# Optimization experiments

Measured on AMD Instinct MI355X. Metric: run time of the kernel, lower is better.

## Reference

```python
import jax, jax.numpy as jnp
import numpy as np

# KernelRnn.slow_update for one converted parameter, time_lag_covariance=None path:
#   var <- variance_update / time_index - mean_update**2
#   update = concat([mean_update, var], axis=0)            # [2R, m, n]
#   val = Q @ update (contract rule axis)                  # [C,  m, n]
#   new_chemical = y*chemical + z*(tanh(K_slow @ chemical) + val)
#   h = v @ new_chemical                                   # [m, n]

C = 5       # numberOfSlowChemicals
R = 14      # numberUpdateRules (all rules enabled)
M, N = 2048, 1024  # underlying weight matrix shape


def setup_inputs() -> dict:
    key = jax.random.key(0)
    ks = jax.random.split(key, 8)
    chemical = jax.random.normal(ks[0], (C, M, N), dtype=jnp.float32)
    mean_update = jax.random.normal(ks[1], (R, M, N), dtype=jnp.float32)
    variance_update = jax.random.uniform(ks[2], (R, M, N), dtype=jnp.float32)
    Q = jax.random.normal(ks[3], (C, 2 * R), dtype=jnp.float32) * 0.01
    K_slow = jax.random.normal(ks[4], (C, C), dtype=jnp.float32) * 0.01
    v = jnp.ones((1, C), dtype=jnp.float32) / C
    # tau-spaced decay vectors as in init_slow_params
    min_tau, max_tau = 2.0, 50.0
    tau = min_tau * (max_tau / min_tau) ** jnp.linspace(0.0, 1.0, C)
    z = (1.0 / tau).astype(jnp.float32)
    y = (1.0 - z).astype(jnp.float32)
    return {
        "chemical": chemical,
        "mean_update": mean_update,
        "variance_update": variance_update,
        "Q": Q,
        "K_slow": K_slow,
        "v": v,
        "y": y,
        "z": z,
        "time_index": 10,
    }


def reference(chemical, mean_update, variance_update, Q, K_slow, v, y, z, time_index):
    inv_t = 1.0 / jnp.asarray(time_index, dtype=chemical.dtype)
    var = variance_update * inv_t - mean_update * mean_update        # [R, m, n]
    update = jnp.concatenate([mean_update, var], axis=0)             # [2R, m, n]
    val = jnp.einsum('cr,rmn->cmn', Q, update)                       # [C, m, n]
    mixed = jnp.tanh(jnp.einsum('cd,dmn->cmn', K_slow, chemical))    # [C, m, n]
    new_chemical = (y[:, None, None] * chemical
                    + z[:, None, None] * (mixed + val))              # [C, m, n]
    h = jnp.einsum('oc,cmn->omn', v, new_chemical)[0]                # [m, n]
    return h
```

## Files before the change

### kernel.cpp

```cpp
#include <hip/hip_runtime.h>


#define CC 5
#define RR 14

__global__ void prep_kernel(const float* __restrict__ Q,
                            const float* __restrict__ Ks,
                            const float* __restrict__ v,
                            const float* __restrict__ y,
                            const float* __restrict__ z,
                            const int* __restrict__ tindex,
                            float* __restrict__ cf) {
    int i = threadIdx.x;
    float inv_t = 1.0f / (float)tindex[0];
    if (i < RR) {
        float a = 0.0f, b = 0.0f;
        #pragma unroll
        for (int c = 0; c < CC; ++c) {
            float vz = v[c] * z[c];
            a = fmaf(vz, Q[c * (2 * RR) + i], a);
            b = fmaf(vz, Q[c * (2 * RR) + RR + i], b);
        }
        cf[i] = a;
        cf[16 + i] = b * inv_t;
        cf[32 + i] = b;
    } else if (i < RR + CC) {
        int c = i - RR;
        cf[48 + c] = v[c] * y[c];
        cf[53 + c] = v[c] * z[c];
    } else if (i < RR + CC + CC * CC) {
        int j = i - (RR + CC);
        cf[58 + j] = Ks[j];
    }
}

__device__ __forceinline__ float fast_tanh(float x) {
    float e = __expf(2.0f * x);
    return fmaf(-2.0f, __builtin_amdgcn_rcpf(e + 1.0f), 1.0f);
}

__global__ __launch_bounds__(256)
void fused_kernel(const float* __restrict__ chem,
                  const float* __restrict__ meanu,
                  const float* __restrict__ varu,
                  const float* __restrict__ cf,
                  float* __restrict__ out,
                  int P) {
    int t = blockIdx.x * blockDim.x + threadIdx.x;
    int p = t * 4;
    if (p >= P) return;

    float4 ch[CC];
    #pragma unroll
    for (int c = 0; c < CC; ++c)
        ch[c] = *reinterpret_cast<const float4*>(chem + (size_t)c * P + p);

    float4 acc = make_float4(0.f, 0.f, 0.f, 0.f);
    #pragma unroll
    for (int c = 0; c < CC; ++c) {
        float vy = cf[48 + c];
        acc.x = fmaf(vy, ch[c].x, acc.x);
        acc.y = fmaf(vy, ch[c].y, acc.y);
        acc.z = fmaf(vy, ch[c].z, acc.z);
        acc.w = fmaf(vy, ch[c].w, acc.w);
    }

    #pragma unroll
    for (int c = 0; c < CC; ++c) {
        float4 s = make_float4(0.f, 0.f, 0.f, 0.f);
        #pragma unroll
        for (int d = 0; d < CC; ++d) {
            float k = cf[58 + c * CC + d];
            s.x = fmaf(k, ch[d].x, s.x);
            s.y = fmaf(k, ch[d].y, s.y);
            s.z = fmaf(k, ch[d].z, s.z);
            s.w = fmaf(k, ch[d].w, s.w);
        }
        float vz = cf[53 + c];
        acc.x = fmaf(vz, fast_tanh(s.x), acc.x);
        acc.y = fmaf(vz, fast_tanh(s.y), acc.y);
        acc.z = fmaf(vz, fast_tanh(s.z), acc.z);
        acc.w = fmaf(vz, fast_tanh(s.w), acc.w);
    }

    #pragma unroll
    for (int r = 0; r < RR; ++r) {
        float4 mu = *reinterpret_cast<const float4*>(meanu + (size_t)r * P + p);
        float4 va = *reinterpret_cast<const float4*>(varu + (size_t)r * P + p);
        float ar = cf[r], bir = cf[16 + r], br = cf[32 + r];
        acc.x = fmaf(ar, mu.x, acc.x);
        acc.y = fmaf(ar, mu.y, acc.y);
        acc.z = fmaf(ar, mu.z, acc.z);
        acc.w = fmaf(ar, mu.w, acc.w);
        acc.x = fmaf(bir, va.x, acc.x);
        acc.y = fmaf(bir, va.y, acc.y);
        acc.z = fmaf(bir, va.z, acc.z);
        acc.w = fmaf(bir, va.w, acc.w);
        acc.x = fmaf(-br, mu.x * mu.x, acc.x);
        acc.y = fmaf(-br, mu.y * mu.y, acc.y);
        acc.z = fmaf(-br, mu.z * mu.z, acc.z);
        acc.w = fmaf(-br, mu.w * mu.w, acc.w);
    }

    *reinterpret_cast<float4*>(out + p) = acc;
}

extern "C" void kernel_launch(void* const* d_in, const int* in_sizes, int n_in,
                              void* d_out, int out_size, void* d_ws, size_t ws_size,
                              hipStream_t stream) {
    const float* chem  = (const float*)d_in[0];
    const float* meanu = (const float*)d_in[1];
    const float* varu  = (const float*)d_in[2];
    const float* Q     = (const float*)d_in[3];
    const float* Ks    = (const float*)d_in[4];
    const float* v     = (const float*)d_in[5];
    const float* y     = (const float*)d_in[6];
    const float* z     = (const float*)d_in[7];
    const int*   ti    = (const int*)d_in[8];

    float* cf = (float*)d_ws;
    float* out = (float*)d_out;

    prep_kernel<<<1, 64, 0, stream>>>(Q, Ks, v, y, z, ti, cf);

    int P = out_size;
    int nthreads = (P + 3) / 4;
    int blocks = (nthreads + 255) / 256;
    fused_kernel<<<blocks, 256, 0, stream>>>(chem, meanu, varu, cf, out, P);
}
```

Baseline: 299.5 us.

## Process two float4 per thread with a rolled update-rule loop

Each thread now handles two float4 vectors, strided by blockDim, and loops over update rules without unrolling. The mean and variance streams are read before the chemical tensor. This is meant to cut register pressure and raise occupancy while keeping coalesced loads. Fewer loads are in flight per thread, and the bounds check is gone, so it relies on P being a multiple of the tile size.

```diff
diff --git a/kernel.cpp b/kernel.cpp
--- a/kernel.cpp
+++ b/kernel.cpp
@@ -3,6 +3,7 @@
 
 #define CC 5
 #define RR 14
+#define VU 2
 
 __global__ void prep_kernel(const float* __restrict__ Q,
                             const float* __restrict__ Ks,
@@ -46,63 +47,80 @@
                   const float* __restrict__ cf,
                   float* __restrict__ out,
                   int P) {
-    int t = blockIdx.x * blockDim.x + threadIdx.x;
-    int p = t * 4;
-    if (p >= P) return;
+    const int tid = threadIdx.x;
+    const size_t tile = (size_t)blockIdx.x * (256 * VU * 4);
 
-    float4 ch[CC];
+    float4 acc[VU];
     #pragma unroll
-    for (int c = 0; c < CC; ++c)
-        ch[c] = *reinterpret_cast<const float4*>(chem + (size_t)c * P + p);
+    for (int u = 0; u < VU; ++u) acc[u] = make_float4(0.f, 0.f, 0.f, 0.f);
 
-    float4 acc = make_float4(0.f, 0.f, 0.f, 0.f);
+    #pragma unroll 1
+    for (int r = 0; r < RR; ++r) {
+        const float4* pm = reinterpret_cast<const float4*>(meanu + (size_t)r * P + tile);
+        const float4* pv = reinterpret_cast<const float4*>(varu  + (size_t)r * P + tile);
+        float4 m[VU], w[VU];
+        #pragma unroll
+        for (int u = 0; u < VU; ++u) m[u] = pm[u * 256 + tid];
+        #pragma unroll
+        for (int u = 0; u < VU; ++u) w[u] = pv[u * 256 + tid];
+        float ar = cf[r], bir = cf[16 + r], br = cf[32 + r];
+        #pragma unroll
+        for (int u = 0; u < VU; ++u) {
+            acc[u].x = fmaf(ar, m[u].x, acc[u].x);
+            acc[u].y = fmaf(ar, m[u].y, acc[u].y);
+            acc[u].z = fmaf(ar, m[u].z, acc[u].z);
+            acc[u].w = fmaf(ar, m[u].w, acc[u].w);
+            acc[u].x = fmaf(bir, w[u].x, acc[u].x);
+            acc[u].y = fmaf(bir, w[u].y, acc[u].y);
+            acc[u].z = fmaf(bir, w[u].z, acc[u].z);
+            acc[u].w = fmaf(bir, w[u].w, acc[u].w);
+            acc[u].x = fmaf(-br, m[u].x * m[u].x, acc[u].x);
+            acc[u].y = fmaf(-br, m[u].y * m[u].y, acc[u].y);
+            acc[u].z = fmaf(-br, m[u].z * m[u].z, acc[u].z);
+            acc[u].w = fmaf(-br, m[u].w * m[u].w, acc[u].w);
+        }
+    }
+
+    float4 ch[CC][VU];
     #pragma unroll
     for (int c = 0; c < CC; ++c) {
-        float vy = cf[48 + c];
-        acc.x = fmaf(vy, ch[c].x, acc.x);
-        acc.y = fmaf(vy, ch[c].y, acc.y);
-        acc.z = fmaf(vy, ch[c].z, acc.z);
-        acc.w = fmaf(vy, ch[c].w, acc.w);
+        const float4* pc = reinterpret_cast<const float4*>(chem + (size_t)c * P + tile);
+        #pragma unroll
+        for (int u = 0; u < VU; ++u) ch[c][u] = pc[u * 256 + tid];
     }
 
     #pragma unroll
-    for (int c = 0; c < CC; ++c) {
-        float4 s = make_float4(0.f, 0.f, 0.f, 0.f);
+    for (int u = 0; u < VU; ++u) {
         #pragma unroll
-        for (int d = 0; d < CC; ++d) {
-            float k = cf[58 + c * CC + d];
-            s.x = fmaf(k, ch[d].x, s.x);
-            s.y = fmaf(k, ch[d].y, s.y);
-            s.z = fmaf(k, ch[d].z, s.z);
-            s.w = fmaf(k, ch[d].w, s.w);
+        for (int c = 0; c < CC; ++c) {
+            float vy = cf[48 + c];
+            acc[u].x = fmaf(vy, ch[c][u].x, acc[u].x);
+            acc[u].y = fmaf(vy, ch[c][u].y, acc[u].y);
+            acc[u].z = fmaf(vy, ch[c][u].z, acc[u].z);
+            acc[u].w = fmaf(vy, ch[c][u].w, acc[u].w);
         }
-        float vz = cf[53 + c];
-        acc.x = fmaf(vz, fast_tanh(s.x), acc.x);
-        acc.y = fmaf(vz, fast_tanh(s.y), acc.y);
-        acc.z = fmaf(vz, fast_tanh(s.z), acc.z);
-        acc.w = fmaf(vz, fast_tanh(s.w), acc.w);
+        #pragma unroll
+        for (int c = 0; c < CC; ++c) {
+            float4 s = make_float4(0.f, 0.f, 0.f, 0.f);
+            #pragma unroll
+            for (int d = 0; d < CC; ++d) {
+                float k = cf[58 + c * CC + d];
+                s.x = fmaf(k, ch[d][u].x, s.x);
+                s.y = fmaf(k, ch[d][u].y, s.y);
+                s.z = fmaf(k, ch[d][u].z, s.z);
+                s.w = fmaf(k, ch[d][u].w, s.w);
+            }
+            float vz = cf[53 + c];
+            acc[u].x = fmaf(vz, fast_tanh(s.x), acc[u].x);
+            acc[u].y = fmaf(vz, fast_tanh(s.y), acc[u].y);
+            acc[u].z = fmaf(vz, fast_tanh(s.z), acc[u].z);
+            acc[u].w = fmaf(vz, fast_tanh(s.w), acc[u].w);
+        }
     }
 
+    float4* po = reinterpret_cast<float4*>(out + tile);
     #pragma unroll
-    for (int r = 0; r < RR; ++r) {
-        float4 mu = *reinterpret_cast<const float4*>(meanu + (size_t)r * P + p);
-        float4 va = *reinterpret_cast<const float4*>(varu + (size_t)r * P + p);
-        float ar = cf[r], bir = cf[16 + r], br = cf[32 + r];
-        acc.x = fmaf(ar, mu.x, acc.x);
-        acc.y = fmaf(ar, mu.y, acc.y);
-        acc.z = fmaf(ar, mu.z, acc.z);
-        acc.w = fmaf(ar, mu.w, acc.w);
-        acc.x = fmaf(bir, va.x, acc.x);
-        acc.y = fmaf(bir, va.y, acc.y);
-        acc.z = fmaf(bir, va.z, acc.z);
-        acc.w = fmaf(bir, va.w, acc.w);
-        acc.x = fmaf(-br, mu.x * mu.x, acc.x);
-        acc.y = fmaf(-br, mu.y * mu.y, acc.y);
-        acc.z = fmaf(-br, mu.z * mu.z, acc.z);
-        acc.w = fmaf(-br, mu.w * mu.w, acc.w);
-    }
-
-    *reinterpret_cast<float4*>(out + p) = acc;
+    for (int u = 0; u < VU; ++u) po[u * 256 + tid] = acc[u];
 }
 
 extern "C" void kernel_launch(void* const* d_in, const int* in_sizes, int n_in,
@@ -124,7 +142,7 @@
     prep_kernel<<<1, 64, 0, stream>>>(Q, Ks, v, y, z, ti, cf);
 
     int P = out_size;
-    int nthreads = (P + 3) / 4;
-    int blocks = (nthreads + 255) / 256;
+    int tile_elems = 256 * VU * 4;
+    int blocks = (P + tile_elems - 1) / tile_elems;
     fused_kernel<<<blocks, 256, 0, stream>>>(chem, meanu, varu, cf, out, P);
 }
```

New measurement: 288.4 us. 1.04x faster.
